# Kernel optimization log

Measured on AMD Instinct MI355X. Metric: run time of the kernel, lower is better.

Reference implementation:

```python
import jax, jax.numpy as jnp
import numpy as np

N, E, EU, L2, EL, G = 50000, 800000, 400000, 131072, 1048576, 512
ND, ED, H, NH, NL, OUT = 128, 16, 128, 4, 2, 1
HD = H // NH


def _ln(x, g, b):
    m = x.mean(-1, keepdims=True)
    v = ((x - m) ** 2).mean(-1, keepdims=True)
    return (x - m) * jax.lax.rsqrt(v + 1e-5) * g + b


def _gcn(x, w, b, ei, n):
    # GCNConv: add self-loops, symmetric normalization, aggregate at ei[1]
    xw = x @ w.T
    loop = jnp.arange(n)
    src = jnp.concatenate([ei[0], loop])
    dst = jnp.concatenate([ei[1], loop])
    deg = jax.ops.segment_sum(jnp.ones_like(src, x.dtype), dst, n)
    dinv = jnp.where(deg > 0, jax.lax.rsqrt(deg), 0.0)
    norm = (dinv[src] * dinv[dst])[:, None]
    return jax.ops.segment_sum(norm * xw[src], dst, n) + b


def _mha(xs, in_w, in_b, out_w, out_b):
    B, S, _ = xs.shape
    qkv = xs @ in_w.T + in_b                       # [B,S,3H]
    q, k, v = jnp.split(qkv, 3, axis=-1)
    hd = lambda a: a.reshape(B, S, NH, HD).transpose(0, 2, 1, 3)
    q, k, v = hd(q), hd(k), hd(v)
    att = jax.nn.softmax(jnp.einsum('bhqd,bhkd->bhqk', q, k) / jnp.sqrt(jnp.float32(HD)), axis=-1)
    o = jnp.einsum('bhqk,bhkd->bhqd', att, v).transpose(0, 2, 1, 3).reshape(B, S, H)
    return o @ out_w.T + out_b


def _encoder(xs, p):
    # torch TransformerEncoderLayer, post-norm, relu activation, dropout=0 (eval)
    for i in range(NL):
        a = _mha(xs, p['in_w'][i], p['in_b'][i], p['out_w'][i], p['out_b'][i])
        xs = _ln(xs + a, p['ln1_g'][i], p['ln1_b'][i])
        ff = jax.nn.relu(xs @ p['ff1_w'][i].T + p['ff1_b'][i]) @ p['ff2_w'][i].T + p['ff2_b'][i]
        xs = _ln(xs + ff, p['ln2_g'][i], p['ln2_b'][i])
    return xs


def _multi_pool(x, idx, g):
    cnt = jax.ops.segment_sum(jnp.ones((x.shape[0],), x.dtype), idx, g)
    mean = jax.ops.segment_sum(x, idx, g) / jnp.maximum(cnt, 1.0)[:, None]
    mx = jax.ops.segment_max(x, idx, g)
    mn = jax.ops.segment_min(x, idx, g)
    mx = jnp.where(jnp.isfinite(mx), mx, 0.0)
    mn = jnp.where(jnp.isfinite(mn), mn, 0.0)
    return jnp.concatenate([mn, mx, mean], axis=-1)


def setup_inputs() -> dict:
    key = jax.random.key(0)
    ks = jax.random.split(key, 40)
    r = lambda i, shape: jax.random.normal(ks[i], shape, jnp.float32) * 0.02
    inp = {}
    inp['x'] = jax.random.normal(ks[0], (N, ND), jnp.float32)
    inp['edge_attr'] = jax.random.normal(ks[1], (EU, ED), jnp.float32)
    inp['edge_index'] = jax.random.randint(ks[2], (2, E), 0, N)
    inp['unique_edges'] = jax.random.randint(ks[3], (2, EU), 0, N)
    inp['batch'] = jnp.sort(jax.random.randint(ks[4], (N,), 0, G))
    inp['l2_node_mapping'] = jax.random.randint(ks[5], (2, L2), 0, EU)
    inp['l2_edge_index'] = jax.random.randint(ks[6], (2, EL), 0, L2)
    inp['num_graphs'] = G
    inp['lin_edge_w'] = r(7, (H, ED)); inp['lin_edge_b'] = jnp.zeros((H,))
    inp['gcn1_w'] = r(8, (H, ND)); inp['gcn1_b'] = jnp.zeros((H,))
    inp['gcn2_w'] = r(9, (H, H)); inp['gcn2_b'] = jnp.zeros((H,))
    inp['t_in_w'] = r(10, (NL, 3 * H, H)); inp['t_in_b'] = jnp.zeros((NL, 3 * H))
    inp['t_out_w'] = r(11, (NL, H, H)); inp['t_out_b'] = jnp.zeros((NL, H))
    inp['t_ln1_g'] = jnp.ones((NL, H)); inp['t_ln1_b'] = jnp.zeros((NL, H))
    inp['t_ln2_g'] = jnp.ones((NL, H)); inp['t_ln2_b'] = jnp.zeros((NL, H))
    inp['t_ff1_w'] = r(12, (NL, 2 * H, H)); inp['t_ff1_b'] = jnp.zeros((NL, 2 * H))
    inp['t_ff2_w'] = r(13, (NL, H, 2 * H)); inp['t_ff2_b'] = jnp.zeros((NL, H))
    inp['f0_w'] = r(14, (H, 9 * H)); inp['f0_b'] = jnp.zeros((H,))
    inp['f0_g'] = jnp.ones((H,)); inp['f0_beta'] = jnp.zeros((H,))
    inp['f1_w'] = r(15, (H, H)); inp['f1_b'] = jnp.zeros((H,))
    inp['f1_g'] = jnp.ones((H,)); inp['f1_beta'] = jnp.zeros((H,))
    inp['fo_w'] = r(16, (OUT, H)); inp['fo_b'] = jnp.zeros((OUT,))
    return inp


def reference(x, edge_attr, lin_edge_w, lin_edge_b, gcn1_w, gcn1_b, gcn2_w, gcn2_b,
              t_in_w, t_in_b, t_out_w, t_out_b, t_ln1_g, t_ln1_b, t_ln2_g, t_ln2_b,
              t_ff1_w, t_ff1_b, t_ff2_w, t_ff2_b, f0_w, f0_b, f0_g, f0_beta,
              f1_w, f1_b, f1_g, f1_beta, fo_w, fo_b,
              edge_index, unique_edges, batch, l2_node_mapping, l2_edge_index, num_graphs):
    H0_edge = edge_attr @ lin_edge_w.T + lin_edge_b                 # [EU,H]
    H0 = _gcn(x, gcn1_w, gcn1_b, edge_index, x.shape[0])            # [N,H]
    e_idx, f_idx = l2_node_mapping[0], l2_node_mapping[1]
    u, v = unique_edges[0, e_idx], unique_edges[1, e_idx]
    s, t = unique_edges[0, f_idx], unique_edges[1, f_idx]
    H0_set = jnp.stack([H0[u], H0[v], H0[s], H0[t], H0_edge[e_idx], H0_edge[f_idx]], axis=1)  # [L2,6,H]
    tp = dict(in_w=t_in_w, in_b=t_in_b, out_w=t_out_w, out_b=t_out_b,
              ln1_g=t_ln1_g, ln1_b=t_ln1_b, ln2_g=t_ln2_g, ln2_b=t_ln2_b,
              ff1_w=t_ff1_w, ff1_b=t_ff1_b, ff2_w=t_ff2_w, ff2_b=t_ff2_b)
    H1 = _encoder(H0_set, tp).mean(axis=1)                          # [L2,H]
    l2_batch = batch[u]
    H2 = jax.nn.relu(_gcn(H1, gcn2_w, gcn2_b, l2_edge_index, H1.shape[0]))
    H0_pool = _multi_pool(H0, batch, num_graphs)
    H1_pool = _multi_pool(H1, l2_batch, num_graphs)
    H2_pool = _multi_pool(H2, l2_batch, num_graphs)
    Hp = jnp.concatenate([H0_pool, H1_pool, H2_pool], axis=1)       # [G,9H]
    h = jax.nn.gelu(_ln(Hp @ f0_w.T + f0_b, f0_g, f0_beta), approximate=False)
    h = jax.nn.gelu(_ln(h @ f1_w.T + f1_b, f1_g, f1_beta), approximate=False)
    return h @ fo_w.T + fo_b
```

## Files before the change

### kernel.cpp

```cpp
#include <hip/hip_runtime.h>

constexpr int cN  = 50000;
constexpr int cE  = 800000;
constexpr int cEU = 400000;
constexpr int cL2 = 131072;
constexpr int cEL = 1048576;
constexpr int cG  = 512;
constexpr int cH  = 128;
constexpr int cNH = 4;
constexpr int cNL = 2;

constexpr int CAP1 = 64;
constexpr int CAP2 = 48;

constexpr int ESETS = 8;
constexpr int ERT   = ESETS * 6;
constexpr int MT    = 3;
constexpr int QS    = 388;
constexpr int AS    = 264;

constexpr int OFF_QKV = 0;
constexpr int OFF_AH  = 74496;
constexpr int OFF_AL  = OFF_AH + 25344;
constexpr int OFF_ATT = OFF_AL + 25344;
constexpr int OFF_IDX = OFF_ATT + 4608;
constexpr int SMEM_SZ = OFF_IDX + 192;

typedef __attribute__((ext_vector_type(8))) short short8v;
typedef __attribute__((ext_vector_type(4))) float f32x4;

#define DEVI __device__ __forceinline__

DEVI unsigned fmap(float x) {
  unsigned u = __float_as_uint(x);
  return (u & 0x80000000u) ? ~u : (u | 0x80000000u);
}
DEVI float funmap(unsigned m) {
  return __uint_as_float((m & 0x80000000u) ? (m & 0x7FFFFFFFu) : ~m);
}
DEVI float gelu_exact(float x) {
  return 0.5f * x * (1.0f + erff(x * 0.70710678118654752f));
}
DEVI unsigned short f2b_rn(float x) {
  unsigned u = __float_as_uint(x);
  return (unsigned short)((u + 0x7FFFu + ((u >> 16) & 1u)) >> 16);
}
DEVI float b2f(unsigned short h) { return __uint_as_float(((unsigned)h) << 16); }
DEVI void sp2(unsigned short* hi, unsigned short* lo, int idx, float a0, float a1) {
  unsigned short h0 = f2b_rn(a0), h1 = f2b_rn(a1);
  unsigned short l0 = f2b_rn(a0 - b2f(h0)), l1 = f2b_rn(a1 - b2f(h1));
  *(unsigned*)&hi[idx] = (unsigned)h0 | ((unsigned)h1 << 16);
  *(unsigned*)&lo[idx] = (unsigned)l0 | ((unsigned)l1 << 16);
}
DEVI void sp4(unsigned short* hi, unsigned short* lo, int idx, float4 v) {
  unsigned short h0 = f2b_rn(v.x), h1 = f2b_rn(v.y), h2 = f2b_rn(v.z), h3 = f2b_rn(v.w);
  unsigned short l0 = f2b_rn(v.x - b2f(h0)), l1 = f2b_rn(v.y - b2f(h1));
  unsigned short l2 = f2b_rn(v.z - b2f(h2)), l3 = f2b_rn(v.w - b2f(h3));
  uint2 H, L;
  H.x = (unsigned)h0 | ((unsigned)h1 << 16);
  H.y = (unsigned)h2 | ((unsigned)h3 << 16);
  L.x = (unsigned)l0 | ((unsigned)l1 << 16);
  L.y = (unsigned)l2 | ((unsigned)l3 << 16);
  *(uint2*)&hi[idx] = H;
  *(uint2*)&lo[idx] = L;
}

__global__ void fill_k(float* p, float v, int n) {
  int i = blockIdx.x * 256 + threadIdx.x;
  if (i < n) p[i] = v;
}

__global__ void deg_count_k(const int* __restrict__ ei, float* deg, int nE) {
  int e = blockIdx.x * 256 + threadIdx.x;
  if (e < nE) atomicAdd(&deg[ei[nE + e]], 1.0f);
}

__global__ void to_dinv_k(float* deg, int n) {
  int i = blockIdx.x * 256 + threadIdx.x;
  if (i < n) deg[i] = rsqrtf(deg[i]);
}

__global__ void csr_fill_k(const int* __restrict__ ei, int* __restrict__ cnt,
                           int* __restrict__ csr, int cap, int nE) {
  int e = blockIdx.x * 256 + threadIdx.x;
  if (e >= nE) return;
  int s = ei[e], d = ei[nE + e];
  int slot = atomicAdd(&cnt[d], 1);
  if (slot < cap) csr[(long)d * cap + slot] = s;
}

__global__ void split_w_k(const float* __restrict__ src, unsigned short* __restrict__ hi,
                          unsigned short* __restrict__ lo, int n) {
  int i = blockIdx.x * 256 + threadIdx.x;
  if (i < n) {
    float x = src[i];
    unsigned short h = f2b_rn(x);
    hi[i] = h;
    lo[i] = f2b_rn(x - b2f(h));
  }
}

__global__ __launch_bounds__(256) void gemm128_k(const float* __restrict__ A,
                                                 const float* __restrict__ W,
                                                 float* __restrict__ C, int M) {
  __shared__ float At[16][132];
  int c = threadIdx.x & 127, rr = threadIdx.x >> 7;
  int base = blockIdx.x * 128;
  for (int tile = 0; tile < 8; ++tile) {
    int r0 = base + tile * 16;
    if (r0 >= M) break;
    __syncthreads();
    for (int i = threadIdx.x; i < 16 * 32; i += 256) {
      int r = i >> 5, s4 = (i & 31) * 4;
      if (r0 + r < M) *(float4*)&At[r][s4] = *(const float4*)&A[(long)(r0 + r) * cH + s4];
    }
    __syncthreads();
    float acc[8];
    #pragma unroll
    for (int j = 0; j < 8; ++j) acc[j] = 0.f;
    const float* wr = W + (long)c * cH;
    for (int k = 0; k < cH; k += 4) {
      float4 w4 = *(const float4*)(wr + k);
      #pragma unroll
      for (int j = 0; j < 8; ++j) {
        float4 a4 = *(const float4*)&At[rr * 8 + j][k];
        acc[j] = fmaf(a4.x, w4.x, acc[j]);
        acc[j] = fmaf(a4.y, w4.y, acc[j]);
        acc[j] = fmaf(a4.z, w4.z, acc[j]);
        acc[j] = fmaf(a4.w, w4.w, acc[j]);
      }
    }
    #pragma unroll
    for (int j = 0; j < 8; ++j) {
      int r = r0 + rr * 8 + j;
      if (r < M) C[(long)r * cH + c] = acc[j];
    }
  }
}

template<int STORE>
__global__ __launch_bounds__(256) void gcn_gather_k(
    const float* __restrict__ xw, const float* __restrict__ dinv,
    const int* __restrict__ csr, const int* __restrict__ cnt,
    const float* __restrict__ bias, float* __restrict__ out,
    const int* __restrict__ gidx,
    float* __restrict__ sum, unsigned* __restrict__ mx, unsigned* __restrict__ mn,
    float* __restrict__ ccnt, int n, int cap) {
  int wv = threadIdx.x >> 6, lane = threadIdx.x & 63;
  int r = blockIdx.x * 4 + wv;
  if (r >= n) return;
  int c = lane * 2;
  float di = dinv[r];
  float2 v0 = *(const float2*)&xw[(long)r * cH + c];
  float2 b2 = *(const float2*)&bias[c];
  float a0 = b2.x + di * di * v0.x;
  float a1 = b2.y + di * di * v0.y;
  int deg = cnt[r];
  if (deg > cap) deg = cap;
  long base = (long)r * cap;
  for (int k = 0; k < deg; ++k) {
    int s = csr[base + k];
    float w = dinv[s] * di;
    float2 v = *(const float2*)&xw[(long)s * cH + c];
    a0 = fmaf(w, v.x, a0);
    a1 = fmaf(w, v.y, a1);
  }
  if (STORE) {
    float2 o; o.x = a0; o.y = a1;
    *(float2*)&out[(long)r * cH + c] = o;
  } else {
    a0 = fmaxf(a0, 0.f);
    a1 = fmaxf(a1, 0.f);
    int g = gidx[r];
    long b = (long)g * cH + c;
    atomicAdd(&sum[b + 0], a0); atomicAdd(&sum[b + 1], a1);
    atomicMax(&mx[b + 0], fmap(a0)); atomicMax(&mx[b + 1], fmap(a1));
    atomicMin(&mn[b + 0], fmap(a0)); atomicMin(&mn[b + 1], fmap(a1));
    if (lane == 0) atomicAdd(&ccnt[g], 1.0f);
  }
}

__global__ __launch_bounds__(512, 1) void encoder_k(
    const float* __restrict__ H0, const float* __restrict__ EA,
    const float* __restrict__ LEW, const float* __restrict__ LEB,
    const int* __restrict__ ue, const int* __restrict__ l2nm,
    const int* __restrict__ batch,
    const unsigned short* __restrict__ WinH, const unsigned short* __restrict__ WinL,
    const float* __restrict__ Bin,
    const unsigned short* __restrict__ WoutH, const unsigned short* __restrict__ WoutL,
    const float* __restrict__ Bout,
    const float* __restrict__ Ln1g, const float* __restrict__ Ln1b,
    const float* __restrict__ Ln2g, const float* __restrict__ Ln2b,
    const unsigned short* __restrict__ Wf1H, const unsigned short* __restrict__ Wf1L,
    const float* __restrict__ Bf1,
    const unsigned short* __restrict__ Wf2H, const unsigned short* __restrict__ Wf2L,
    const float* __restrict__ Bf2,
    float* __restrict__ H1,
    float* __restrict__ sum1, unsigned* __restrict__ mx1, unsigned* __restrict__ mn1,
    float* __restrict__ cnt1, int* __restrict__ l2b) {
  extern __shared__ char smem[];
  float* QKV = (float*)(smem + OFF_QKV);
  unsigned short* Ahs = (unsigned short*)(smem + OFF_AH);
  unsigned short* Als = (unsigned short*)(smem + OFF_AL);
  float* att = (float*)(smem + OFF_ATT);
  int* nidx = (int*)(smem + OFF_IDX);
  int* eidx = nidx + 32;

  const int tid = threadIdx.x;
  const int lane = tid & 63, wv = tid >> 6;
  const int lr = lane & 15, lq = lane >> 4;
  const int base = blockIdx.x * ESETS;

  if (tid < ESETS) {
    int e = l2nm[base + tid];
    int f = l2nm[cL2 + base + tid];
    eidx[tid * 2 + 0] = e;
    eidx[tid * 2 + 1] = f;
    nidx[tid * 4 + 0] = ue[e];
    nidx[tid * 4 + 1] = ue[cEU + e];
    nidx[tid * 4 + 2] = ue[f];
    nidx[tid * 4 + 3] = ue[cEU + f];
  }
  __syncthreads();
  for (int i = tid; i < 32 * 32; i += 512) {
    int q = i >> 5, s4 = (i & 31) * 4;
    int r = (q >> 2) * 6 + (q & 3);
    float4 v = *(const float4*)&H0[(long)nidx[q] * cH + s4];
    sp4(Ahs, Als, r * AS + s4, v);
  }
  for (int i = tid; i < ESETS * cH; i += 512) {
    int c = (i & 63) * 2, q = i >> 6;
    const float* row = EA + (long)eidx[q] * 16;
    const float* w0 = LEW + c * 16;
    const float* w1 = LEW + (c + 1) * 16;
    float2 bb2 = *(const float2*)&LEB[c];
    float a0 = bb2.x, a1 = bb2.y;
    #pragma unroll
    for (int d = 0; d < 16; ++d) {
      float rv = row[d];
      a0 = fmaf(rv, w0[d], a0);
      a1 = fmaf(rv, w1[d], a1);
    }
    int r = (q >> 1) * 6 + 4 + (q & 1);
    sp2(Ahs, Als, r * AS + c, a0, a1);
  }
  __syncthreads();

  for (int l = 0; l < cNL; ++l) {
    {
      const unsigned short* WH = WinH + (long)l * 384 * 128;
      const unsigned short* WL = WinL + (long)l * 384 * 128;
      const float* BB = Bin + l * 384;
      #pragma unroll
      for (int ni = 0; ni < 3; ++ni) {
        int col = (wv + 8 * ni) * 16 + lr;
        const unsigned short* wp = WH + (long)col * 128 + (lq << 3);
        const unsigned short* wq = WL + (long)col * 128 + (lq << 3);
        f32x4 accH[MT], accL1[MT], accL2[MT];
        #pragma unroll
        for (int m = 0; m < MT; ++m) {
          accH[m] = (f32x4){0.f, 0.f, 0.f, 0.f};
          accL1[m] = (f32x4){0.f, 0.f, 0.f, 0.f};
          accL2[m] = (f32x4){0.f, 0.f, 0.f, 0.f};
        }
        #pragma unroll
        for (int ks = 0; ks < 4; ++ks) {
          short8v bh = *(const short8v*)&wp[ks * 32];
          short8v bl = *(const short8v*)&wq[ks * 32];
          #pragma unroll
          for (int m = 0; m < MT; ++m) {
            int ao = (m * 16 + lr) * AS + (lq << 3) + ks * 32;
            short8v ah = *(const short8v*)&Ahs[ao];
            short8v al = *(const short8v*)&Als[ao];
            accL1[m] = __builtin_amdgcn_mfma_f32_16x16x32_bf16(al, bh, accL1[m], 0, 0, 0);
            accL2[m] = __builtin_amdgcn_mfma_f32_16x16x32_bf16(ah, bl, accL2[m], 0, 0, 0);
            accH[m] = __builtin_amdgcn_mfma_f32_16x16x32_bf16(ah, bh, accH[m], 0, 0, 0);
          }
        }
        float bv = BB[col];
        #pragma unroll
        for (int m = 0; m < MT; ++m) {
          int r0 = m * 16 + (lq << 2);
          #pragma unroll
          for (int j = 0; j < 4; ++j)
            QKV[(r0 + j) * QS + col] = accH[m][j] + (accL1[m][j] + accL2[m][j]) + bv;
        }
      }
    }
    __syncthreads();
    {
      const int s = wv;
      float* attS = att + s * 144;
      if (lane < 24) {
        int h = lane / 6, qt = lane % 6;
        const float* qp = &QKV[(s * 6 + qt) * QS + h * 32];
        float4 qv[8];
        #pragma unroll
        for (int j4 = 0; j4 < 8; ++j4) qv[j4] = *(const float4*)&qp[j4 * 4];
        float sc[6];
        #pragma unroll
        for (int kt = 0; kt < 6; ++kt) {
          const float* kp = &QKV[(s * 6 + kt) * QS + 128 + h * 32];
          float d = 0.f;
          #pragma unroll
          for (int j4 = 0; j4 < 8; ++j4) {
            float4 b4 = *(const float4*)&kp[j4 * 4];
            d = fmaf(qv[j4].x, b4.x, d); d = fmaf(qv[j4].y, b4.y, d);
            d = fmaf(qv[j4].z, b4.z, d); d = fmaf(qv[j4].w, b4.w, d);
          }
          sc[kt] = d * 0.17677669529663687f;
        }
        float mx = sc[0];
        #pragma unroll
        for (int kt = 1; kt < 6; ++kt) mx = fmaxf(mx, sc[kt]);
        float ev[6]; float sum = 0.f;
        #pragma unroll
        for (int kt = 0; kt < 6; ++kt) { ev[kt] = expf(sc[kt] - mx); sum += ev[kt]; }
        float inv = 1.f / sum;
        #pragma unroll
        for (int kt = 0; kt < 6; ++kt) attS[(h * 6 + qt) * 6 + kt] = ev[kt] * inv;
      }
      asm volatile("s_waitcnt lgkmcnt(0)" ::: "memory");
      __builtin_amdgcn_sched_barrier(0);
      {
        int c = lane * 2;
        int h = c >> 5;
        #pragma unroll
        for (int r = 0; r < 6; ++r) {
          const float* arow = &attS[(h * 6 + r) * 6];
          float d0 = 0.f, d1 = 0.f;
          #pragma unroll
          for (int kt = 0; kt < 6; ++kt) {
            float2 v2 = *(const float2*)&QKV[(s * 6 + kt) * QS + 256 + c];
            float a = arow[kt];
            d0 = fmaf(a, v2.x, d0);
            d1 = fmaf(a, v2.y, d1);
          }
          sp2(Ahs, Als, (s * 6 + r) * AS + 128 + c, d0, d1);
        }
      }
    }
    __syncthreads();
    {
      const unsigned short* WH = WoutH + (long)l * 128 * 128;
      const unsigned short* WL = WoutL + (long)l * 128 * 128;
      int col = wv * 16 + lr;
      const unsigned short* wp = WH + (long)col * 128 + (lq << 3);
      const unsigned short* wq = WL + (long)col * 128 + (lq << 3);
      f32x4 accH[MT], accL1[MT], accL2[MT];
      #pragma unroll
      for (int m = 0; m < MT; ++m) {
        accH[m] = (f32x4){0.f, 0.f, 0.f, 0.f};
        accL1[m] = (f32x4){0.f, 0.f, 0.f, 0.f};
        accL2[m] = (f32x4){0.f, 0.f, 0.f, 0.f};
      }
      #pragma unroll
      for (int ks = 0; ks < 4; ++ks) {
        short8v bh = *(const short8v*)&wp[ks * 32];
        short8v bl = *(const short8v*)&wq[ks * 32];
        #pragma unroll
        for (int m = 0; m < MT; ++m) {
          int ao = (m * 16 + lr) * AS + 128 + (lq << 3) + ks * 32;
          short8v ah = *(const short8v*)&Ahs[ao];
          short8v al = *(const short8v*)&Als[ao];
          accL1[m] = __builtin_amdgcn_mfma_f32_16x16x32_bf16(al, bh, accL1[m], 0, 0, 0);
          accL2[m] = __builtin_amdgcn_mfma_f32_16x16x32_bf16(ah, bl, accL2[m], 0, 0, 0);
          accH[m] = __builtin_amdgcn_mfma_f32_16x16x32_bf16(ah, bh, accH[m], 0, 0, 0);
        }
      }
      float bv = Bout[l * 128 + col];
      #pragma unroll
      for (int m = 0; m < MT; ++m) {
        int r0 = m * 16 + (lq << 2);
        #pragma unroll
        for (int j = 0; j < 4; ++j)
          QKV[(r0 + j) * QS + col] = accH[m][j] + (accL1[m][j] + accL2[m][j]) + bv;
      }
    }
    __syncthreads();
    {
      const float* gg = Ln1g + l * cH;
      const float* bb = Ln1b + l * cH;
      #pragma unroll
      for (int p = 0; p < MT; ++p) {
        int r = p * 16 + (tid >> 5);
        int c0 = (tid & 31) * 4;
        ushort4 ah4 = *(const ushort4*)&Ahs[r * AS + c0];
        ushort4 al4 = *(const ushort4*)&Als[r * AS + c0];
        float4 q4 = *(const float4*)&QKV[r * QS + c0];
        float y[4];
        y[0] = b2f(ah4.x) + b2f(al4.x) + q4.x;
        y[1] = b2f(ah4.y) + b2f(al4.y) + q4.y;
        y[2] = b2f(ah4.z) + b2f(al4.z) + q4.z;
        y[3] = b2f(ah4.w) + b2f(al4.w) + q4.w;
        float s = 0.f, s2 = 0.f;
        #pragma unroll
        for (int j = 0; j < 4; ++j) { s += y[j]; s2 += y[j] * y[j]; }
        #pragma unroll
        for (int m = 1; m < 32; m <<= 1) { s += __shfl_xor(s, m, 32); s2 += __shfl_xor(s2, m, 32); }
        float mean = s * (1.f / 128.f);
        float rstd = rsqrtf(s2 * (1.f / 128.f) - mean * mean + 1e-5f);
        float4 g4 = *(const float4*)&gg[c0];
        float4 b4v = *(const float4*)&bb[c0];
        float4 xn4;
        xn4.x = (y[0] - mean) * rstd * g4.x + b4v.x;
        xn4.y = (y[1] - mean) * rstd * g4.y + b4v.y;
        xn4.z = (y[2] - mean) * rstd * g4.z + b4v.z;
        xn4.w = (y[3] - mean) * rstd * g4.w + b4v.w;
        *(float4*)&QKV[r * QS + 128 + c0] = xn4;
        sp4(Ahs, Als, r * AS + c0, xn4);
      }
    }
    __syncthreads();
    {
      const unsigned short* WH = Wf1H + (long)l * 256 * 128;
      const unsigned short* WL = Wf1L + (long)l * 256 * 128;
      #pragma unroll
      for (int ni = 0; ni < 2; ++ni) {
        int col = (wv + 8 * ni) * 16 + lr;
        const unsigned short* wp = WH + (long)col * 128 + (lq << 3);
        const unsigned short* wq = WL + (long)col * 128 + (lq << 3);
        f32x4 accH[MT], accL1[MT], accL2[MT];
        #pragma unroll
        for (int m = 0; m < MT; ++m) {
          accH[m] = (f32x4){0.f, 0.f, 0.f, 0.f};
          accL1[m] = (f32x4){0.f, 0.f, 0.f, 0.f};
          accL2[m] = (f32x4){0.f, 0.f, 0.f, 0.f};
        }
        #pragma unroll
        for (int ks = 0; ks < 4; ++ks) {
          short8v bh = *(const short8v*)&wp[ks * 32];
          short8v bl = *(const short8v*)&wq[ks * 32];
          #pragma unroll
          for (int m = 0; m < MT; ++m) {
            int ao = (m * 16 + lr) * AS + (lq << 3) + ks * 32;
            short8v ah = *(const short8v*)&Ahs[ao];
            short8v al = *(const short8v*)&Als[ao];
            accL1[m] = __builtin_amdgcn_mfma_f32_16x16x32_bf16(al, bh, accL1[m], 0, 0, 0);
            accL2[m] = __builtin_amdgcn_mfma_f32_16x16x32_bf16(ah, bl, accL2[m], 0, 0, 0);
            accH[m] = __builtin_amdgcn_mfma_f32_16x16x32_bf16(ah, bh, accH[m], 0, 0, 0);
          }
        }
        int lc = col + (col >= 128 ? 128 : 0);
        #pragma unroll
        for (int m = 0; m < MT; ++m) {
          int r0 = m * 16 + (lq << 2);
          #pragma unroll
          for (int j = 0; j < 4; ++j)
            QKV[(r0 + j) * QS + lc] = accH[m][j] + (accL1[m][j] + accL2[m][j]);
        }
      }
    }
    __syncthreads();
    for (int i = tid; i < ERT * 128; i += 512) {
      int r = i >> 7, n = (i & 127) * 2;
      int lc = n + (n >= 128 ? 128 : 0);
      float2 v2 = *(const float2*)&QKV[r * QS + lc];
      float2 bb2 = *(const float2*)&Bf1[l * 256 + n];
      float h0 = fmaxf(v2.x + bb2.x, 0.f);
      float h1 = fmaxf(v2.y + bb2.y, 0.f);
      sp2(Ahs, Als, r * AS + n, h0, h1);
    }
    __syncthreads();
    {
      const unsigned short* WH = Wf2H + (long)l * 128 * 256;
      const unsigned short* WL = Wf2L + (long)l * 128 * 256;
      int col = wv * 16 + lr;
      const unsigned short* wp = WH + (long)col * 256 + (lq << 3);
      const unsigned short* wq = WL + (long)col * 256 + (lq << 3);
      f32x4 accH[MT], accL1[MT], accL2[MT];
      #pragma unroll
      for (int m = 0; m < MT; ++m) {
        accH[m] = (f32x4){0.f, 0.f, 0.f, 0.f};
        accL1[m] = (f32x4){0.f, 0.f, 0.f, 0.f};
        accL2[m] = (f32x4){0.f, 0.f, 0.f, 0.f};
      }
      #pragma unroll
      for (int ks = 0; ks < 8; ++ks) {
        short8v bh = *(const short8v*)&wp[ks * 32];
        short8v bl = *(const short8v*)&wq[ks * 32];
        #pragma unroll
        for (int m = 0; m < MT; ++m) {
          int ao = (m * 16 + lr) * AS + (lq << 3) + ks * 32;
          short8v ah = *(const short8v*)&Ahs[ao];
          short8v al = *(const short8v*)&Als[ao];
          accL1[m] = __builtin_amdgcn_mfma_f32_16x16x32_bf16(al, bh, accL1[m], 0, 0, 0);
          accL2[m] = __builtin_amdgcn_mfma_f32_16x16x32_bf16(ah, bl, accL2[m], 0, 0, 0);
          accH[m] = __builtin_amdgcn_mfma_f32_16x16x32_bf16(ah, bh, accH[m], 0, 0, 0);
        }
      }
      float bv = Bf2[l * 128 + col];
      #pragma unroll
      for (int m = 0; m < MT; ++m) {
        int r0 = m * 16 + (lq << 2);
        #pragma unroll
        for (int j = 0; j < 4; ++j)
          QKV[(r0 + j) * QS + col] = accH[m][j] + (accL1[m][j] + accL2[m][j]) + bv;
      }
    }
    __syncthreads();
    {
      const float* gg = Ln2g + l * cH;
      const float* bb = Ln2b + l * cH;
      #pragma unroll
      for (int p = 0; p < MT; ++p) {
        int r = p * 16 + (tid >> 5);
        int c0 = (tid & 31) * 4;
        float4 qa = *(const float4*)&QKV[r * QS + 128 + c0];
        float4 qb = *(const float4*)&QKV[r * QS + c0];
        float y[4];
        y[0] = qa.x + qb.x; y[1] = qa.y + qb.y;
        y[2] = qa.z + qb.z; y[3] = qa.w + qb.w;
        float s = 0.f, s2 = 0.f;
        #pragma unroll
        for (int j = 0; j < 4; ++j) { s += y[j]; s2 += y[j] * y[j]; }
        #pragma unroll
        for (int m = 1; m < 32; m <<= 1) { s += __shfl_xor(s, m, 32); s2 += __shfl_xor(s2, m, 32); }
        float mean = s * (1.f / 128.f);
        float rstd = rsqrtf(s2 * (1.f / 128.f) - mean * mean + 1e-5f);
        float4 g4 = *(const float4*)&gg[c0];
        float4 b4v = *(const float4*)&bb[c0];
        float4 xn4;
        xn4.x = (y[0] - mean) * rstd * g4.x + b4v.x;
        xn4.y = (y[1] - mean) * rstd * g4.y + b4v.y;
        xn4.z = (y[2] - mean) * rstd * g4.z + b4v.z;
        xn4.w = (y[3] - mean) * rstd * g4.w + b4v.w;
        sp4(Ahs, Als, r * AS + c0, xn4);
      }
    }
    __syncthreads();
  }

  {
    int s = tid >> 6, c = (tid & 63) * 2;
    float m0 = 0.f, m1 = 0.f;
    #pragma unroll
    for (int t = 0; t < 6; ++t) {
      unsigned hh = *(const unsigned*)&Ahs[(s * 6 + t) * AS + c];
      unsigned ll = *(const unsigned*)&Als[(s * 6 + t) * AS + c];
      m0 += b2f((unsigned short)(hh & 0xFFFFu)) + b2f((unsigned short)(ll & 0xFFFFu));
      m1 += b2f((unsigned short)(hh >> 16)) + b2f((unsigned short)(ll >> 16));
    }
    float v0 = m0 * (1.f / 6.f), v1 = m1 * (1.f / 6.f);
    float2 o; o.x = v0; o.y = v1;
    *(float2*)&H1[(long)(base + s) * cH + c] = o;
    int g = batch[nidx[s * 4]];
    long b = (long)g * cH + c;
    atomicAdd(&sum1[b + 0], v0);  atomicAdd(&sum1[b + 1], v1);
    atomicMax(&mx1[b + 0], fmap(v0)); atomicMax(&mx1[b + 1], fmap(v1));
    atomicMin(&mn1[b + 0], fmap(v0)); atomicMin(&mn1[b + 1], fmap(v1));
    if (c == 0) {
      atomicAdd(&cnt1[g], 1.0f);
      l2b[base + s] = g;
    }
  }
}

__global__ void init_stats3_k(char* ST, size_t stride) {
  int i = blockIdx.x * 256 + threadIdx.x;
  if (i >= cG * cH) return;
  #pragma unroll
  for (int p = 0; p < 3; ++p) {
    char* b = ST + (size_t)p * stride;
    ((float*)b)[i] = 0.f;
    ((unsigned*)(b + (size_t)cG * cH * 4))[i] = 0u;
    ((unsigned*)(b + (size_t)cG * cH * 8))[i] = 0xFFFFFFFFu;
    if (i < cG) ((float*)(b + (size_t)cG * cH * 12))[i] = 0.f;
  }
}

__global__ void pool_sorted_k(const float* __restrict__ X, const int* __restrict__ gidx,
                              float* sum, unsigned* mx, unsigned* mn, float* cnt, int n) {
  long t = (long)blockIdx.x * 256 + threadIdx.x;
  int q = (int)(t & 31) * 4;
  long r0 = (t >> 5) * 8;
  if (r0 >= n) return;
  int gcur = -1;
  float s0 = 0, s1 = 0, s2 = 0, s3 = 0, cc = 0;
  float x0 = 0, x1 = 0, x2 = 0, x3 = 0;
  float n0 = 0, n1 = 0, n2 = 0, n3 = 0;
  for (int k = 0; k < 8; ++k) {
    long r = r0 + k;
    if (r >= n) break;
    int g = gidx[r];
    float4 v = *(const float4*)&X[r * cH + q];
    if (g != gcur) {
// ... 150 lines not shown
  const float* tf2w  = (const float*)d_in[24];
  const float* tf2b  = (const float*)d_in[25];
  const float* f0w   = (const float*)d_in[26];
  const float* f0b   = (const float*)d_in[27];
  const float* f0g   = (const float*)d_in[28];
  const float* f0bb  = (const float*)d_in[29];
  const float* f1w   = (const float*)d_in[30];
  const float* f1b   = (const float*)d_in[31];
  const float* f1g   = (const float*)d_in[32];
  const float* f1bb  = (const float*)d_in[33];
  const float* fow   = (const float*)d_in[34];
  const float* fob   = (const float*)d_in[35];
  float* out = (float*)d_out;

  char* ws = (char*)d_ws;
  size_t off = 0;
  float* H1  = (float*)(ws + off);  off += (size_t)cL2 * cH * 4;
  float* H0  = (float*)(ws + off);  off += (size_t)cL2 * cH * 4;
  float* XW  = (float*)(ws + off);  off += (size_t)cL2 * cH * 4;
  float* DEG = (float*)(ws + off);  off += (size_t)cL2 * 4;
  int*   L2B = (int*)(ws + off);    off += (size_t)cL2 * 4;
  int*   CNT = (int*)(ws + off);    off += (size_t)cL2 * 4;
  char*  ST  = ws + off;            off += 3 * ((size_t)cG * cH * 4 * 3 + cG * 4);
  int*   CSR1 = (int*)(ws + off);   off += (size_t)cN * CAP1 * 4;
  int*   CSR2 = (int*)(ws + off);   off += (size_t)cL2 * CAP2 * 4;
  unsigned short* WinH  = (unsigned short*)(ws + off); off += (size_t)cNL * 384 * 128 * 2;
  unsigned short* WinL  = (unsigned short*)(ws + off); off += (size_t)cNL * 384 * 128 * 2;
  unsigned short* WoutH = (unsigned short*)(ws + off); off += (size_t)cNL * 128 * 128 * 2;
  unsigned short* WoutL = (unsigned short*)(ws + off); off += (size_t)cNL * 128 * 128 * 2;
  unsigned short* Wf1H  = (unsigned short*)(ws + off); off += (size_t)cNL * 256 * 128 * 2;
  unsigned short* Wf1L  = (unsigned short*)(ws + off); off += (size_t)cNL * 256 * 128 * 2;
  unsigned short* Wf2H  = (unsigned short*)(ws + off); off += (size_t)cNL * 128 * 256 * 2;
  unsigned short* Wf2L  = (unsigned short*)(ws + off); off += (size_t)cNL * 128 * 256 * 2;

  size_t st_stride = (size_t)cG * cH * 4 * 3 + cG * 4;
  auto stat = [&](int p) {
    char* b = ST + p * st_stride;
    struct S { float* sum; unsigned* mx; unsigned* mn; float* cnt; } s;
    s.sum = (float*)b;
    s.mx  = (unsigned*)(b + (size_t)cG * cH * 4);
    s.mn  = (unsigned*)(b + (size_t)cG * cH * 8);
    s.cnt = (float*)(b + (size_t)cG * cH * 12);
    return s;
  };
  auto s0 = stat(0), s1 = stat(1), s2 = stat(2);

  split_w_k<<<(cNL * 384 * 128 + 255) / 256, 256, 0, stream>>>(tinw, WinH, WinL, cNL * 384 * 128);
  split_w_k<<<(cNL * 128 * 128 + 255) / 256, 256, 0, stream>>>(toutw, WoutH, WoutL, cNL * 128 * 128);
  split_w_k<<<(cNL * 256 * 128 + 255) / 256, 256, 0, stream>>>(tf1w, Wf1H, Wf1L, cNL * 256 * 128);
  split_w_k<<<(cNL * 128 * 256 + 255) / 256, 256, 0, stream>>>(tf2w, Wf2H, Wf2L, cNL * 128 * 256);
  init_stats3_k<<<(cG * cH + 255) / 256, 256, 0, stream>>>(ST, st_stride);

  gemm128_k<<<(cN + 127) / 128, 256, 0, stream>>>(x, g1w, XW, cN);
  fill_k<<<(cN + 255) / 256, 256, 0, stream>>>(DEG, 1.0f, cN);
  deg_count_k<<<(cE + 255) / 256, 256, 0, stream>>>(ei, DEG, cE);
  to_dinv_k<<<(cN + 255) / 256, 256, 0, stream>>>(DEG, cN);
  fill_k<<<(cN + 255) / 256, 256, 0, stream>>>((float*)CNT, 0.0f, cN);
  csr_fill_k<<<(cE + 255) / 256, 256, 0, stream>>>(ei, CNT, CSR1, CAP1, cE);
  gcn_gather_k<1><<<(cN + 3) / 4, 256, 0, stream>>>(XW, DEG, CSR1, CNT, g1b, H0,
      nullptr, nullptr, nullptr, nullptr, nullptr, cN, CAP1);

  hipFuncSetAttribute(reinterpret_cast<const void*>(encoder_k),
                      hipFuncAttributeMaxDynamicSharedMemorySize, 131072);
  encoder_k<<<cL2 / ESETS, 512, SMEM_SZ, stream>>>(H0, ea, lew, leb, ue, l2nm, batch,
      WinH, WinL, tinb, WoutH, WoutL, toutb, tl1g, tl1b, tl2g, tl2b,
      Wf1H, Wf1L, tf1b, Wf2H, Wf2L, tf2b, H1,
      s1.sum, s1.mx, s1.mn, s1.cnt, L2B);

  pool_sorted_k<<<(int)((((long)(cN + 7) / 8) * 32 + 255) / 256), 256, 0, stream>>>(
      H0, batch, s0.sum, s0.mx, s0.mn, s0.cnt, cN);

  gemm128_k<<<(cL2 + 127) / 128, 256, 0, stream>>>(H1, g2w, XW, cL2);
  fill_k<<<(cL2 + 255) / 256, 256, 0, stream>>>(DEG, 1.0f, cL2);
  deg_count_k<<<(cEL + 255) / 256, 256, 0, stream>>>(l2ei, DEG, cEL);
  to_dinv_k<<<(cL2 + 255) / 256, 256, 0, stream>>>(DEG, cL2);
  fill_k<<<(cL2 + 255) / 256, 256, 0, stream>>>((float*)CNT, 0.0f, cL2);
  csr_fill_k<<<(cEL + 255) / 256, 256, 0, stream>>>(l2ei, CNT, CSR2, CAP2, cEL);
  gcn_gather_k<0><<<(cL2 + 3) / 4, 256, 0, stream>>>(XW, DEG, CSR2, CNT, g2b, nullptr,
      L2B, s2.sum, s2.mx, s2.mn, s2.cnt, cL2, CAP2);

  mlp_k<<<cG, 128, 0, stream>>>(ST, st_stride, f0w, f0b, f0g, f0bb, f1w, f1b, f1g, f1bb, fow, fob, out);
}
```

Before: 4.360 ms.

## Double encoder block to 1024 threads and derive GCN degree from CSR counts

The encoder kernel now runs 16 waves per block instead of 8. The row tiles of each GEMM are split between two wave groups (32 rows and 16 rows), and the attention softmax and AV stages are split across those groups. The aim is more latency hiding inside each block, at the cost of an extra barrier and an uneven MFMA load between the two groups. Separately, the degree atomic pass is removed and dinv is computed from the in-degree counts that csr_fill already produces, which drops two kernels and one atomic scatter per GCN layer.

```diff
diff --git a/kernel.cpp b/kernel.cpp
--- a/kernel.cpp
+++ b/kernel.cpp
@@ -15,7 +15,6 @@
 
 constexpr int ESETS = 8;
 constexpr int ERT   = ESETS * 6;
-constexpr int MT    = 3;
 constexpr int QS    = 388;
 constexpr int AS    = 264;
 
@@ -65,19 +64,49 @@
   *(uint2*)&lo[idx] = L;
 }
 
+template<int MCNT, int NKS>
+DEVI void mfma_gemm(const unsigned short* __restrict__ Ahs,
+                    const unsigned short* __restrict__ Als,
+                    int abase,
+                    const unsigned short* __restrict__ wp,
+                    const unsigned short* __restrict__ wq,
+                    f32x4* acc) {
+  f32x4 aH[MCNT], a1[MCNT], a2[MCNT];
+  #pragma unroll
+  for (int mi = 0; mi < MCNT; ++mi) {
+    aH[mi] = (f32x4){0.f, 0.f, 0.f, 0.f};
+    a1[mi] = (f32x4){0.f, 0.f, 0.f, 0.f};
+    a2[mi] = (f32x4){0.f, 0.f, 0.f, 0.f};
+  }
+  #pragma unroll
+  for (int ks = 0; ks < NKS; ++ks) {
+    short8v bh = *(const short8v*)&wp[ks * 32];
+    short8v bl = *(const short8v*)&wq[ks * 32];
+    #pragma unroll
+    for (int mi = 0; mi < MCNT; ++mi) {
+      int ao = abase + mi * (16 * AS) + ks * 32;
+      short8v ah = *(const short8v*)&Ahs[ao];
+      short8v al = *(const short8v*)&Als[ao];
+      a1[mi] = __builtin_amdgcn_mfma_f32_16x16x32_bf16(al, bh, a1[mi], 0, 0, 0);
+      a2[mi] = __builtin_amdgcn_mfma_f32_16x16x32_bf16(ah, bl, a2[mi], 0, 0, 0);
+      aH[mi] = __builtin_amdgcn_mfma_f32_16x16x32_bf16(ah, bh, aH[mi], 0, 0, 0);
+    }
+  }
+  #pragma unroll
+  for (int mi = 0; mi < MCNT; ++mi) {
+    #pragma unroll
+    for (int j = 0; j < 4; ++j) acc[mi][j] = aH[mi][j] + (a1[mi][j] + a2[mi][j]);
+  }
+}
+
 __global__ void fill_k(float* p, float v, int n) {
   int i = blockIdx.x * 256 + threadIdx.x;
   if (i < n) p[i] = v;
 }
 
-__global__ void deg_count_k(const int* __restrict__ ei, float* deg, int nE) {
-  int e = blockIdx.x * 256 + threadIdx.x;
-  if (e < nE) atomicAdd(&deg[ei[nE + e]], 1.0f);
-}
-
-__global__ void to_dinv_k(float* deg, int n) {
+__global__ void cnt_to_dinv_k(const int* __restrict__ cnt, float* __restrict__ dinv, int n) {
   int i = blockIdx.x * 256 + threadIdx.x;
-  if (i < n) deg[i] = rsqrtf(deg[i]);
+  if (i < n) dinv[i] = rsqrtf((float)cnt[i] + 1.0f);
 }
 
 __global__ void csr_fill_k(const int* __restrict__ ei, int* __restrict__ cnt,
@@ -180,7 +209,7 @@
   }
 }
 
-__global__ __launch_bounds__(512, 1) void encoder_k(
+__global__ __launch_bounds__(1024, 1) void encoder_k(
     const float* __restrict__ H0, const float* __restrict__ EA,
     const float* __restrict__ LEW, const float* __restrict__ LEB,
     const int* __restrict__ ue, const int* __restrict__ l2nm,
@@ -209,6 +238,7 @@
   const int tid = threadIdx.x;
   const int lane = tid & 63, wv = tid >> 6;
   const int lr = lane & 15, lq = lane >> 4;
+  const int cw = wv & 7, mg = wv >> 3;
   const int base = blockIdx.x * ESETS;
 
   if (tid < ESETS) {
@@ -222,13 +252,15 @@
     nidx[tid * 4 + 3] = ue[cEU + f];
   }
   __syncthreads();
-  for (int i = tid; i < 32 * 32; i += 512) {
+  {
+    int i = tid;
     int q = i >> 5, s4 = (i & 31) * 4;
     int r = (q >> 2) * 6 + (q & 3);
     float4 v = *(const float4*)&H0[(long)nidx[q] * cH + s4];
     sp4(Ahs, Als, r * AS + s4, v);
   }
-  for (int i = tid; i < ESETS * cH; i += 512) {
+  {
+    int i = tid;
     int c = (i & 63) * 2, q = i >> 6;
     const float* row = EA + (long)eidx[q] * 16;
     const float* w0 = LEW + c * 16;
@@ -253,46 +285,34 @@
       const float* BB = Bin + l * 384;
       #pragma unroll
       for (int ni = 0; ni < 3; ++ni) {
-        int col = (wv + 8 * ni) * 16 + lr;
+        int col = (cw + 8 * ni) * 16 + lr;
         const unsigned short* wp = WH + (long)col * 128 + (lq << 3);
         const unsigned short* wq = WL + (long)col * 128 + (lq << 3);
-        f32x4 accH[MT], accL1[MT], accL2[MT];
-        #pragma unroll
-        for (int m = 0; m < MT; ++m) {
-          accH[m] = (f32x4){0.f, 0.f, 0.f, 0.f};
-          accL1[m] = (f32x4){0.f, 0.f, 0.f, 0.f};
-          accL2[m] = (f32x4){0.f, 0.f, 0.f, 0.f};
+        float bv = BB[col];
+        if (mg == 0) {
+          f32x4 acc[2];
+          mfma_gemm<2, 4>(Ahs, Als, lr * AS + (lq << 3), wp, wq, acc);
+          #pragma unroll
+          for (int mi = 0; mi < 2; ++mi) {
+            int r0 = mi * 16 + (lq << 2);
+            #pragma unroll
+            for (int j = 0; j < 4; ++j) QKV[(r0 + j) * QS + col] = acc[mi][j] + bv;
+          }
+        } else {
+          f32x4 acc[1];
+          mfma_gemm<1, 4>(Ahs, Als, (32 + lr) * AS + (lq << 3), wp, wq, acc);
+          int r0 = 32 + (lq << 2);
+          #pragma unroll
+          for (int j = 0; j < 4; ++j) QKV[(r0 + j) * QS + col] = acc[0][j] + bv;
         }
-        #pragma unroll
-        for (int ks = 0; ks < 4; ++ks) {
-          short8v bh = *(const short8v*)&wp[ks * 32];
-          short8v bl = *(const short8v*)&wq[ks * 32];
-          #pragma unroll
-          for (int m = 0; m < MT; ++m) {
-            int ao = (m * 16 + lr) * AS + (lq << 3) + ks * 32;
-            short8v ah = *(const short8v*)&Ahs[ao];
-            short8v al = *(const short8v*)&Als[ao];
-            accL1[m] = __builtin_amdgcn_mfma_f32_16x16x32_bf16(al, bh, accL1[m], 0, 0, 0);
-            accL2[m] = __builtin_amdgcn_mfma_f32_16x16x32_bf16(ah, bl, accL2[m], 0, 0, 0);
-            accH[m] = __builtin_amdgcn_mfma_f32_16x16x32_bf16(ah, bh, accH[m], 0, 0, 0);
-          }
-        }
-        float bv = BB[col];
-        #pragma unroll
-        for (int m = 0; m < MT; ++m) {
-          int r0 = m * 16 + (lq << 2);
-          #pragma unroll
-          for (int j = 0; j < 4; ++j)
-            QKV[(r0 + j) * QS + col] = accH[m][j] + (accL1[m][j] + accL2[m][j]) + bv;
-        }
       }
     }
     __syncthreads();
     {
-      const int s = wv;
+      const int s = cw;
       float* attS = att + s * 144;
-      if (lane < 24) {
-        int h = lane / 6, qt = lane % 6;
+      if (lane < 12) {
+        int h = mg * 2 + lane / 6, qt = lane % 6;
         const float* qp = &QKV[(s * 6 + qt) * QS + h * 32];
         float4 qv[8];
         #pragma unroll
@@ -320,61 +340,51 @@
         #pragma unroll
         for (int kt = 0; kt < 6; ++kt) attS[(h * 6 + qt) * 6 + kt] = ev[kt] * inv;
       }
-      asm volatile("s_waitcnt lgkmcnt(0)" ::: "memory");
-      __builtin_amdgcn_sched_barrier(0);
-      {
-        int c = lane * 2;
-        int h = c >> 5;
-        #pragma unroll
-        for (int r = 0; r < 6; ++r) {
-          const float* arow = &attS[(h * 6 + r) * 6];
-          float d0 = 0.f, d1 = 0.f;
-          #pragma unroll
-          for (int kt = 0; kt < 6; ++kt) {
-            float2 v2 = *(const float2*)&QKV[(s * 6 + kt) * QS + 256 + c];
-            float a = arow[kt];
-            d0 = fmaf(a, v2.x, d0);
-            d1 = fmaf(a, v2.y, d1);
-          }
-          sp2(Ahs, Als, (s * 6 + r) * AS + 128 + c, d0, d1);
+    }
+    __syncthreads();
+    {
+      const int s = cw;
+      float* attS = att + s * 144;
+      int c = lane * 2;
+      int h = c >> 5;
+      #pragma unroll
+      for (int ri = 0; ri < 3; ++ri) {
+        int r = mg * 3 + ri;
+        const float* arow = &attS[(h * 6 + r) * 6];
+        float d0 = 0.f, d1 = 0.f;
+        #pragma unroll
+        for (int kt = 0; kt < 6; ++kt) {
+          float2 v2 = *(const float2*)&QKV[(s * 6 + kt) * QS + 256 + c];
+          float a = arow[kt];
+          d0 = fmaf(a, v2.x, d0);
+          d1 = fmaf(a, v2.y, d1);
         }
+        sp2(Ahs, Als, (s * 6 + r) * AS + 128 + c, d0, d1);
       }
     }
     __syncthreads();
     {
       const unsigned short* WH = WoutH + (long)l * 128 * 128;
       const unsigned short* WL = WoutL + (long)l * 128 * 128;
-      int col = wv * 16 + lr;
+      int col = cw * 16 + lr;
       const unsigned short* wp = WH + (long)col * 128 + (lq << 3);
       const unsigned short* wq = WL + (long)col * 128 + (lq << 3);
-      f32x4 accH[MT], accL1[MT], accL2[MT];
-      #pragma unroll
-      for (int m = 0; m < MT; ++m) {
-        accH[m] = (f32x4){0.f, 0.f, 0.f, 0.f};
-        accL1[m] = (f32x4){0.f, 0.f, 0.f, 0.f};
-        accL2[m] = (f32x4){0.f, 0.f, 0.f, 0.f};
-      }
-      #pragma unroll
-      for (int ks = 0; ks < 4; ++ks) {
-        short8v bh = *(const short8v*)&wp[ks * 32];
-        short8v bl = *(const short8v*)&wq[ks * 32];
-        #pragma unroll
-        for (int m = 0; m < MT; ++m) {
-          int ao = (m * 16 + lr) * AS + 128 + (lq << 3) + ks * 32;
-          short8v ah = *(const short8v*)&Ahs[ao];
-          short8v al = *(const short8v*)&Als[ao];
-          accL1[m] = __builtin_amdgcn_mfma_f32_16x16x32_bf16(al, bh, accL1[m], 0, 0, 0);
-          accL2[m] = __builtin_amdgcn_mfma_f32_16x16x32_bf16(ah, bl, accL2[m], 0, 0, 0);
-          accH[m] = __builtin_amdgcn_mfma_f32_16x16x32_bf16(ah, bh, accH[m], 0, 0, 0);
+      float bv = Bout[l * 128 + col];
+      if (mg == 0) {
+        f32x4 acc[2];
+        mfma_gemm<2, 4>(Ahs, Als, lr * AS + 128 + (lq << 3), wp, wq, acc);
+        #pragma unroll
+        for (int mi = 0; mi < 2; ++mi) {
+          int r0 = mi * 16 + (lq << 2);
+          #pragma unroll
+          for (int j = 0; j < 4; ++j) QKV[(r0 + j) * QS + col] = acc[mi][j] + bv;
         }
-      }
-      float bv = Bout[l * 128 + col];
-      #pragma unroll
-      for (int m = 0; m < MT; ++m) {
-        int r0 = m * 16 + (lq << 2);
-        #pragma unroll
-        for (int j = 0; j < 4; ++j)
-          QKV[(r0 + j) * QS + col] = accH[m][j] + (accL1[m][j] + accL2[m][j]) + bv;
+      } else {
+        f32x4 acc[1];
+        mfma_gemm<1, 4>(Ahs, Als, (32 + lr) * AS + 128 + (lq << 3), wp, wq, acc);
+        int r0 = 32 + (lq << 2);
+        #pragma unroll
+        for (int j = 0; j < 4; ++j) QKV[(r0 + j) * QS + col] = acc[0][j] + bv;
       }
     }
     __syncthreads();
@@ -382,33 +392,35 @@
       const float* gg = Ln1g + l * cH;
       const float* bb = Ln1b + l * cH;
       #pragma unroll
-      for (int p = 0; p < MT; ++p) {
-        int r = p * 16 + (tid >> 5);
-        int c0 = (tid & 31) * 4;
-        ushort4 ah4 = *(const ushort4*)&Ahs[r * AS + c0];
-        ushort4 al4 = *(const ushort4*)&Als[r * AS + c0];
-        float4 q4 = *(const float4*)&QKV[r * QS + c0];
-        float y[4];
-        y[0] = b2f(ah4.x) + b2f(al4.x) + q4.x;
-        y[1] = b2f(ah4.y) + b2f(al4.y) + q4.y;
-        y[2] = b2f(ah4.z) + b2f(al4.z) + q4.z;
-        y[3] = b2f(ah4.w) + b2f(al4.w) + q4.w;
-        float s = 0.f, s2 = 0.f;
-        #pragma unroll
-        for (int j = 0; j < 4; ++j) { s += y[j]; s2 += y[j] * y[j]; }
-        #pragma unroll
-        for (int m = 1; m < 32; m <<= 1) { s += __shfl_xor(s, m, 32); s2 += __shfl_xor(s2, m, 32); }
-        float mean = s * (1.f / 128.f);
-        float rstd = rsqrtf(s2 * (1.f / 128.f) - mean * mean + 1e-5f);
-        float4 g4 = *(const float4*)&gg[c0];
-        float4 b4v = *(const float4*)&bb[c0];
-        float4 xn4;
-        xn4.x = (y[0] - mean) * rstd * g4.x + b4v.x;
-        xn4.y = (y[1] - mean) * rstd * g4.y + b4v.y;
-        xn4.z = (y[2] - mean) * rstd * g4.z + b4v.z;
-        xn4.w = (y[3] - mean) * rstd * g4.w + b4v.w;
-        *(float4*)&QKV[r * QS + 128 + c0] = xn4;
-        sp4(Ahs, Als, r * AS + c0, xn4);
+      for (int p = 0; p < 2; ++p) {
+        int r = p * 32 + (tid >> 5);
+        if (r < ERT) {
+          int c0 = (tid & 31) * 4;
+          ushort4 ah4 = *(const ushort4*)&Ahs[r * AS + c0];
+          ushort4 al4 = *(const ushort4*)&Als[r * AS + c0];
+          float4 q4 = *(const float4*)&QKV[r * QS + c0];
+          float y[4];
+          y[0] = b2f(ah4.x) + b2f(al4.x) + q4.x;
+          y[1] = b2f(ah4.y) + b2f(al4.y) + q4.y;
+          y[2] = b2f(ah4.z) + b2f(al4.z) + q4.z;
+          y[3] = b2f(ah4.w) + b2f(al4.w) + q4.w;
+          float s = 0.f, s2 = 0.f;
+          #pragma unroll
+          for (int j = 0; j < 4; ++j) { s += y[j]; s2 += y[j] * y[j]; }
+          #pragma unroll
+          for (int m = 1; m < 32; m <<= 1) { s += __shfl_xor(s, m, 32); s2 += __shfl_xor(s2, m, 32); }
+          float mean = s * (1.f / 128.f);
+          float rstd = rsqrtf(s2 * (1.f / 128.f) - mean * mean + 1e-5f);
+          float4 g4 = *(const float4*)&gg[c0];
+          float4 b4v = *(const float4*)&bb[c0];
+          float4 xn4;
+          xn4.x = (y[0] - mean) * rstd * g4.x + b4v.x;
+          xn4.y = (y[1] - mean) * rstd * g4.y + b4v.y;
+          xn4.z = (y[2] - mean) * rstd * g4.z + b4v.z;
+          xn4.w = (y[3] - mean) * rstd * g4.w + b4v.w;
+          *(float4*)&QKV[r * QS + 128 + c0] = xn4;
+          sp4(Ahs, Als, r * AS + c0, xn4);
+        }
       }
     }
     __syncthreads();
@@ -417,42 +429,30 @@
       const unsigned short* WL = Wf1L + (long)l * 256 * 128;
       #pragma unroll
       for (int ni = 0; ni < 2; ++ni) {
-        int col = (wv + 8 * ni) * 16 + lr;
+        int col = (cw + 8 * ni) * 16 + lr;
         const unsigned short* wp = WH + (long)col * 128 + (lq << 3);
         const unsigned short* wq = WL + (long)col * 128 + (lq << 3);
-        f32x4 accH[MT], accL1[MT], accL2[MT];
-        #pragma unroll
-        for (int m = 0; m < MT; ++m) {
-          accH[m] = (f32x4){0.f, 0.f, 0.f, 0.f};
-          accL1[m] = (f32x4){0.f, 0.f, 0.f, 0.f};
-          accL2[m] = (f32x4){0.f, 0.f, 0.f, 0.f};
+        int lc = col + (col >= 128 ? 128 : 0);
+        if (mg == 0) {
+          f32x4 acc[2];
+          mfma_gemm<2, 4>(Ahs, Als, lr * AS + (lq << 3), wp, wq, acc);
+          #pragma unroll
+          for (int mi = 0; mi < 2; ++mi) {
+            int r0 = mi * 16 + (lq << 2);
+            #pragma unroll
+            for (int j = 0; j < 4; ++j) QKV[(r0 + j) * QS + lc] = acc[mi][j];
+          }
+        } else {
+          f32x4 acc[1];
+          mfma_gemm<1, 4>(Ahs, Als, (32 + lr) * AS + (lq << 3), wp, wq, acc);
+          int r0 = 32 + (lq << 2);
+          #pragma unroll
+          for (int j = 0; j < 4; ++j) QKV[(r0 + j) * QS + lc] = acc[0][j];
         }
-        #pragma unroll
-        for (int ks = 0; ks < 4; ++ks) {
-          short8v bh = *(const short8v*)&wp[ks * 32];
-          short8v bl = *(const short8v*)&wq[ks * 32];
-          #pragma unroll
-          for (int m = 0; m < MT; ++m) {
-            int ao = (m * 16 + lr) * AS + (lq << 3) + ks * 32;
-            short8v ah = *(const short8v*)&Ahs[ao];
-            short8v al = *(const short8v*)&Als[ao];
-            accL1[m] = __builtin_amdgcn_mfma_f32_16x16x32_bf16(al, bh, accL1[m], 0, 0, 0);
-            accL2[m] = __builtin_amdgcn_mfma_f32_16x16x32_bf16(ah, bl, accL2[m], 0, 0, 0);
-            accH[m] = __builtin_amdgcn_mfma_f32_16x16x32_bf16(ah, bh, accH[m], 0, 0, 0);
-          }
-        }
-        int lc = col + (col >= 128 ? 128 : 0);
-        #pragma unroll
-        for (int m = 0; m < MT; ++m) {
-          int r0 = m * 16 + (lq << 2);
-          #pragma unroll
-          for (int j = 0; j < 4; ++j)
-            QKV[(r0 + j) * QS + lc] = accH[m][j] + (accL1[m][j] + accL2[m][j]);
-        }
-      }
-    }
-    __syncthreads();
-    for (int i = tid; i < ERT * 128; i += 512) {
+      }
+    }
+    __syncthreads();
+    for (int i = tid; i < ERT * 128; i += 1024) {
       int r = i >> 7, n = (i & 127) * 2;
       int lc = n + (n >= 128 ? 128 : 0);
       float2 v2 = *(const float2*)&QKV[r * QS + lc];
@@ -465,37 +465,25 @@
     {
       const unsigned short* WH = Wf2H + (long)l * 128 * 256;
       const unsigned short* WL = Wf2L + (long)l * 128 * 256;
-      int col = wv * 16 + lr;
+      int col = cw * 16 + lr;
       const unsigned short* wp = WH + (long)col * 256 + (lq << 3);
       const unsigned short* wq = WL + (long)col * 256 + (lq << 3);
-      f32x4 accH[MT], accL1[MT], accL2[MT];
-      #pragma unroll
-      for (int m = 0; m < MT; ++m) {
-        accH[m] = (f32x4){0.f, 0.f, 0.f, 0.f};
-        accL1[m] = (f32x4){0.f, 0.f, 0.f, 0.f};
-        accL2[m] = (f32x4){0.f, 0.f, 0.f, 0.f};
-      }
-      #pragma unroll
-      for (int ks = 0; ks < 8; ++ks) {
-        short8v bh = *(const short8v*)&wp[ks * 32];
-        short8v bl = *(const short8v*)&wq[ks * 32];
-        #pragma unroll
-        for (int m = 0; m < MT; ++m) {
-          int ao = (m * 16 + lr) * AS + (lq << 3) + ks * 32;
-          short8v ah = *(const short8v*)&Ahs[ao];
-          short8v al = *(const short8v*)&Als[ao];
-          accL1[m] = __builtin_amdgcn_mfma_f32_16x16x32_bf16(al, bh, accL1[m], 0, 0, 0);
-          accL2[m] = __builtin_amdgcn_mfma_f32_16x16x32_bf16(ah, bl, accL2[m], 0, 0, 0);
-          accH[m] = __builtin_amdgcn_mfma_f32_16x16x32_bf16(ah, bh, accH[m], 0, 0, 0);
+      float bv = Bf2[l * 128 + col];
+      if (mg == 0) {
+        f32x4 acc[2];
+        mfma_gemm<2, 8>(Ahs, Als, lr * AS + (lq << 3), wp, wq, acc);
+        #pragma unroll
+        for (int mi = 0; mi < 2; ++mi) {
+          int r0 = mi * 16 + (lq << 2);
+          #pragma unroll
+          for (int j = 0; j < 4; ++j) QKV[(r0 + j) * QS + col] = acc[mi][j] + bv;
         }
-      }
-      float bv = Bf2[l * 128 + col];
-      #pragma unroll
-      for (int m = 0; m < MT; ++m) {
-        int r0 = m * 16 + (lq << 2);
-        #pragma unroll
-        for (int j = 0; j < 4; ++j)
-          QKV[(r0 + j) * QS + col] = accH[m][j] + (accL1[m][j] + accL2[m][j]) + bv;
+      } else {
+        f32x4 acc[1];
+        mfma_gemm<1, 8>(Ahs, Als, (32 + lr) * AS + (lq << 3), wp, wq, acc);
+        int r0 = 32 + (lq << 2);
+        #pragma unroll
+        for (int j = 0; j < 4; ++j) QKV[(r0 + j) * QS + col] = acc[0][j] + bv;
       }
     }
     __syncthreads();
@@ -503,35 +491,37 @@
       const float* gg = Ln2g + l * cH;
       const float* bb = Ln2b + l * cH;
       #pragma unroll
-      for (int p = 0; p < MT; ++p) {
-        int r = p * 16 + (tid >> 5);
-        int c0 = (tid & 31) * 4;
-        float4 qa = *(const float4*)&QKV[r * QS + 128 + c0];
-        float4 qb = *(const float4*)&QKV[r * QS + c0];
-        float y[4];
-        y[0] = qa.x + qb.x; y[1] = qa.y + qb.y;
-        y[2] = qa.z + qb.z; y[3] = qa.w + qb.w;
-        float s = 0.f, s2 = 0.f;
-        #pragma unroll
-        for (int j = 0; j < 4; ++j) { s += y[j]; s2 += y[j] * y[j]; }
-        #pragma unroll
-        for (int m = 1; m < 32; m <<= 1) { s += __shfl_xor(s, m, 32); s2 += __shfl_xor(s2, m, 32); }
-        float mean = s * (1.f / 128.f);
-        float rstd = rsqrtf(s2 * (1.f / 128.f) - mean * mean + 1e-5f);
-        float4 g4 = *(const float4*)&gg[c0];
-        float4 b4v = *(const float4*)&bb[c0];
-        float4 xn4;
-        xn4.x = (y[0] - mean) * rstd * g4.x + b4v.x;
-        xn4.y = (y[1] - mean) * rstd * g4.y + b4v.y;
-        xn4.z = (y[2] - mean) * rstd * g4.z + b4v.z;
-        xn4.w = (y[3] - mean) * rstd * g4.w + b4v.w;
-        sp4(Ahs, Als, r * AS + c0, xn4);
-      }
-    }
-    __syncthreads();
-  }
-
-  {
+      for (int p = 0; p < 2; ++p) {
+        int r = p * 32 + (tid >> 5);
+        if (r < ERT) {
+          int c0 = (tid & 31) * 4;
+          float4 qa = *(const float4*)&QKV[r * QS + 128 + c0];
+          float4 qb = *(const float4*)&QKV[r * QS + c0];
+          float y[4];
+          y[0] = qa.x + qb.x; y[1] = qa.y + qb.y;
+          y[2] = qa.z + qb.z; y[3] = qa.w + qb.w;
+          float s = 0.f, s2 = 0.f;
+          #pragma unroll
+          for (int j = 0; j < 4; ++j) { s += y[j]; s2 += y[j] * y[j]; }
+          #pragma unroll
+          for (int m = 1; m < 32; m <<= 1) { s += __shfl_xor(s, m, 32); s2 += __shfl_xor(s2, m, 32); }
+          float mean = s * (1.f / 128.f);
+          float rstd = rsqrtf(s2 * (1.f / 128.f) - mean * mean + 1e-5f);
+          float4 g4 = *(const float4*)&gg[c0];
+          float4 b4v = *(const float4*)&bb[c0];
+          float4 xn4;
+          xn4.x = (y[0] - mean) * rstd * g4.x + b4v.x;
+          xn4.y = (y[1] - mean) * rstd * g4.y + b4v.y;
+          xn4.z = (y[2] - mean) * rstd * g4.z + b4v.z;
+          xn4.w = (y[3] - mean) * rstd * g4.w + b4v.w;
+          sp4(Ahs, Als, r * AS + c0, xn4);
+        }
+      }
+    }
+    __syncthreads();
+  }
+
+  if (tid < ESETS * 64) {
     int s = tid >> 6, c = (tid & 63) * 2;
     float m0 = 0.f, m1 = 0.f;
     #pragma unroll
@@ -788,17 +778,15 @@
   init_stats3_k<<<(cG * cH + 255) / 256, 256, 0, stream>>>(ST, st_stride);
 
   gemm128_k<<<(cN + 127) / 128, 256, 0, stream>>>(x, g1w, XW, cN);
-  fill_k<<<(cN + 255) / 256, 256, 0, stream>>>(DEG, 1.0f, cN);
-  deg_count_k<<<(cE + 255) / 256, 256, 0, stream>>>(ei, DEG, cE);
-  to_dinv_k<<<(cN + 255) / 256, 256, 0, stream>>>(DEG, cN);
   fill_k<<<(cN + 255) / 256, 256, 0, stream>>>((float*)CNT, 0.0f, cN);
   csr_fill_k<<<(cE + 255) / 256, 256, 0, stream>>>(ei, CNT, CSR1, CAP1, cE);
+  cnt_to_dinv_k<<<(cN + 255) / 256, 256, 0, stream>>>(CNT, DEG, cN);
   gcn_gather_k<1><<<(cN + 3) / 4, 256, 0, stream>>>(XW, DEG, CSR1, CNT, g1b, H0,
       nullptr, nullptr, nullptr, nullptr, nullptr, cN, CAP1);
 
   hipFuncSetAttribute(reinterpret_cast<const void*>(encoder_k),
                       hipFuncAttributeMaxDynamicSharedMemorySize, 131072);
-  encoder_k<<<cL2 / ESETS, 512, SMEM_SZ, stream>>>(H0, ea, lew, leb, ue, l2nm, batch,
+  encoder_k<<<cL2 / ESETS, 1024, SMEM_SZ, stream>>>(H0, ea, lew, leb, ue, l2nm, batch,
       WinH, WinL, tinb, WoutH, WoutL, toutb, tl1g, tl1b, tl2g, tl2b,
       Wf1H, Wf1L, tf1b, Wf2H, Wf2L, tf2b, H1,
       s1.sum, s1.mx, s1.mn, s1.cnt, L2B);
@@ -807,11 +795,9 @@
       H0, batch, s0.sum, s0.mx, s0.mn, s0.cnt, cN);
 
   gemm128_k<<<(cL2 + 127) / 128, 256, 0, stream>>>(H1, g2w, XW, cL2);
-  fill_k<<<(cL2 + 255) / 256, 256, 0, stream>>>(DEG, 1.0f, cL2);
-  deg_count_k<<<(cEL + 255) / 256, 256, 0, stream>>>(l2ei, DEG, cEL);
-  to_dinv_k<<<(cL2 + 255) / 256, 256, 0, stream>>>(DEG, cL2);
   fill_k<<<(cL2 + 255) / 256, 256, 0, stream>>>((float*)CNT, 0.0f, cL2);
   csr_fill_k<<<(cEL + 255) / 256, 256, 0, stream>>>(l2ei, CNT, CSR2, CAP2, cEL);
+  cnt_to_dinv_k<<<(cL2 + 255) / 256, 256, 0, stream>>>(CNT, DEG, cL2);
   gcn_gather_k<0><<<(cL2 + 3) / 4, 256, 0, stream>>>(XW, DEG, CSR2, CNT, g2b, nullptr,
       L2B, s2.sum, s2.mx, s2.mn, s2.cnt, cL2, CAP2);
 
```

Measured after the change: 6.802 ms. 1.56x slower.
